# Kernel optimization log

Hardware: AMD Instinct MI355X
Metric: run time of the kernel (lower is better)

## Reference

```python
import jax, jax.numpy as jnp
import numpy as np

B, S = 4096, 4096
NEG_INF = -1e30


def _conv1d_same(x, w, pad):
    # x: [B, S], w: [K] -> cross-correlation with zero padding, like torch F.conv1d
    out = jax.lax.conv_general_dilated(
        x[:, None, :], w[None, None, :], (1,), [(pad, pad)],
        dimension_numbers=("NCH", "OIH", "NCH"))
    return out[:, 0, :]


def setup_inputs() -> dict:
    key = jax.random.key(0)
    kx, kl, k1, k2, k3 = jax.random.split(key, 5)
    x = jax.random.normal(kx, (B, S), dtype=jnp.float32)
    length = jax.random.randint(kl, (B,), 1, S + 1, dtype=jnp.int32)
    w1 = 0.01 * jax.random.normal(k1, (3,), dtype=jnp.float32)
    w2 = 0.01 * jax.random.normal(k2, (5,), dtype=jnp.float32)
    w3 = 0.01 * jax.random.normal(k3, (7,), dtype=jnp.float32)
    return {"x": x, "length": length, "w1": w1, "w2": w2, "w3": w3}


def reference(x, length, w1, w2, w3):
    # mask out padding beyond each sample's length; zeroing x beyond length makes
    # the 'same'-padded conv identical to per-sample conv on the truncated sequence
    pos = jnp.arange(S)
    mask = pos[None, :] < length[:, None]          # [B, S]
    xm = jnp.where(mask, x, 0.0)

    def branch(w, pad):
        logits = _conv1d_same(xm, w, pad)          # [B, S]
        logits = jnp.where(mask, logits, NEG_INF)  # softmax only over valid positions
        qw = jax.nn.softmax(logits, axis=-1)
        return jnp.sum(qw * xm, axis=-1)           # [B]

    s1 = branch(w1, 1)
    s2 = branch(w2, 2)
    s3 = branch(w3, 3)
    fused = (s1 + s2 + s3) / 3.0
    return fused[:, None]                          # [B, 1]
```

## Files before the change

kernel.cpp:

```cpp
#include <hip/hip_runtime.h>

#define SEQ 4096
#define NTHREADS 256

__global__ __launch_bounds__(NTHREADS) void msr_kernel(
    const float* __restrict__ x, const int* __restrict__ length,
    const float* __restrict__ w1, const float* __restrict__ w2,
    const float* __restrict__ w3, float* __restrict__ out)
{
    __shared__ float sm[SEQ + 8];
    __shared__ float red[4][8];

    const int row = blockIdx.x;
    const int tid = threadIdx.x;
    const int L   = length[row];

    const float a0 = w1[0], a1 = w1[1], a2 = w1[2];
    const float b0 = w2[0], b1 = w2[1], b2 = w2[2], b3 = w2[3], b4 = w2[4];
    const float c0 = w3[0], c1 = w3[1], c2 = w3[2], c3 = w3[3],
                c4 = w3[4], c5 = w3[5], c6 = w3[6];

    if (tid < 4) { sm[tid] = 0.0f; sm[4 + SEQ + tid] = 0.0f; }

    const float4* xrow = reinterpret_cast<const float4*>(x + (size_t)row * SEQ);
    for (int q = tid; q < SEQ / 4; q += NTHREADS) {
        const int e = q * 4;
        float4 v;
        if (e + 3 < L) {
            v = xrow[q];
        } else if (e < L) {
            v = xrow[q];
            if (e + 1 >= L) v.y = 0.0f;
            if (e + 2 >= L) v.z = 0.0f;
            v.w = 0.0f;
        } else {
            v = make_float4(0.0f, 0.0f, 0.0f, 0.0f);
        }
        *reinterpret_cast<float4*>(&sm[4 + e]) = v;
    }
    __syncthreads();

    float d1 = 0.f, n1 = 0.f, d2 = 0.f, n2 = 0.f, d3 = 0.f, n3 = 0.f;
    for (int i = tid; i < L; i += NTHREADS) {
        const float* p = &sm[4 + i];
        const float vm3 = p[-3], vm2 = p[-2], vm1 = p[-1], v0 = p[0],
                    vp1 = p[1],  vp2 = p[2],  vp3 = p[3];
        const float l1 = a0*vm1 + a1*v0 + a2*vp1;
        const float l2 = b0*vm2 + b1*vm1 + b2*v0 + b3*vp1 + b4*vp2;
        const float l3 = c0*vm3 + c1*vm2 + c2*vm1 + c3*v0 + c4*vp1 + c5*vp2 + c6*vp3;
        const float e1 = __expf(l1), e2 = __expf(l2), e3 = __expf(l3);
        d1 += e1; n1 = fmaf(e1, v0, n1);
        d2 += e2; n2 = fmaf(e2, v0, n2);
        d3 += e3; n3 = fmaf(e3, v0, n3);
    }

    #pragma unroll
    for (int off = 32; off > 0; off >>= 1) {
        d1 += __shfl_down(d1, off);
        n1 += __shfl_down(n1, off);
        d2 += __shfl_down(d2, off);
        n2 += __shfl_down(n2, off);
        d3 += __shfl_down(d3, off);
        n3 += __shfl_down(n3, off);
    }
    const int wave = tid >> 6;
    const int lane = tid & 63;
    if (lane == 0) {
        red[wave][0] = d1; red[wave][1] = n1; red[wave][2] = d2;
        red[wave][3] = n2; red[wave][4] = d3; red[wave][5] = n3;
    }
    __syncthreads();
    if (tid == 0) {
        float D1 = 0.f, N1 = 0.f, D2 = 0.f, N2 = 0.f, D3 = 0.f, N3 = 0.f;
        #pragma unroll
        for (int w = 0; w < NTHREADS / 64; ++w) {
            D1 += red[w][0]; N1 += red[w][1]; D2 += red[w][2];
            N2 += red[w][3]; D3 += red[w][4]; N3 += red[w][5];
        }
        const float s1 = N1 / D1, s2 = N2 / D2, s3 = N3 / D3;
        out[row] = (s1 + s2 + s3) * (1.0f / 3.0f);
    }
}

extern "C" void kernel_launch(void* const* d_in, const int* in_sizes, int n_in,
                              void* d_out, int out_size, void* d_ws, size_t ws_size,
                              hipStream_t stream) {
    const float* x      = (const float*)d_in[0];
    const int*   length = (const int*)d_in[1];
    const float* w1     = (const float*)d_in[2];
    const float* w2     = (const float*)d_in[3];
    const float* w3     = (const float*)d_in[4];
    float*       out    = (float*)d_out;
    const int    Bn     = in_sizes[1];
    msr_kernel<<<Bn, NTHREADS, 0, stream>>>(x, length, w1, w2, w3, out);
}
```

Measured before the change: 21.96 us.

## Use one wavefront per row with register stencil via lane shuffles

Replaces the 256-thread block that staged the row in LDS with a single 64-lane wave per row that streams 256-element chunks in registers. Conv halos are exchanged with lane shuffles and carried between chunks, and loads are software-pipelined two chunks ahead. Full chunks skip masking, and the shared-memory reduction and barriers go away. In exchange each row is now handled serially by one wave, which lowers per-row parallelism and leans on memory-level parallelism across many small blocks.

New measurement: 21.53 us. 2.0% less time.

```diff
diff --git a/kernel.cpp b/kernel.cpp
--- a/kernel.cpp
+++ b/kernel.cpp
@@ -1,84 +1,107 @@
 #include <hip/hip_runtime.h>
+#include <type_traits>
 
 #define SEQ 4096
-#define NTHREADS 256
+#define CHUNK 256
 
-__global__ __launch_bounds__(NTHREADS) void msr_kernel(
+__global__ __launch_bounds__(64) void msr_kernel(
     const float* __restrict__ x, const int* __restrict__ length,
     const float* __restrict__ w1, const float* __restrict__ w2,
     const float* __restrict__ w3, float* __restrict__ out)
 {
-    __shared__ float sm[SEQ + 8];
-    __shared__ float red[4][8];
+    const int row  = blockIdx.x;
+    const int lane = threadIdx.x & 63;
+    const int L    = length[row];
 
-    const int row = blockIdx.x;
-    const int tid = threadIdx.x;
-    const int L   = length[row];
+    const float a0=w1[0],a1=w1[1],a2=w1[2];
+    const float b0=w2[0],b1=w2[1],b2=w2[2],b3=w2[3],b4=w2[4];
+    const float c0=w3[0],c1=w3[1],c2=w3[2],c3=w3[3],c4=w3[4],c5=w3[5],c6=w3[6];
 
-    const float a0 = w1[0], a1 = w1[1], a2 = w1[2];
-    const float b0 = w2[0], b1 = w2[1], b2 = w2[2], b3 = w2[3], b4 = w2[4];
-    const float c0 = w3[0], c1 = w3[1], c2 = w3[2], c3 = w3[3],
-                c4 = w3[4], c5 = w3[5], c6 = w3[6];
+    const float4* __restrict__ xrow =
+        reinterpret_cast<const float4*>(x + (size_t)row * SEQ);
 
-    if (tid < 4) { sm[tid] = 0.0f; sm[4 + SEQ + tid] = 0.0f; }
+    float d1=0.f,n1=0.f,d2=0.f,n2=0.f,d3=0.f,n3=0.f;
+    float cax=0.f, cay=0.f, caz=0.f;
 
-    const float4* xrow = reinterpret_cast<const float4*>(x + (size_t)row * SEQ);
-    for (int q = tid; q < SEQ / 4; q += NTHREADS) {
-        const int e = q * 4;
-        float4 v;
-        if (e + 3 < L) {
-            v = xrow[q];
-        } else if (e < L) {
-            v = xrow[q];
-            if (e + 1 >= L) v.y = 0.0f;
-            if (e + 2 >= L) v.z = 0.0f;
-            v.w = 0.0f;
-        } else {
-            v = make_float4(0.0f, 0.0f, 0.0f, 0.0f);
+    auto load_chunk = [&](int it) -> float4 {
+        float4 v = make_float4(0.f,0.f,0.f,0.f);
+        const int start = it * CHUNK;
+        if (start < L) {
+            if (start + CHUNK <= L) {
+                v = xrow[(it << 6) + lane];
+            } else {
+                const int e = start + (lane << 2);
+                if (e < L) {
+                    v = xrow[(it << 6) + lane];
+                    if (e + 1 >= L) v.y = 0.f;
+                    if (e + 2 >= L) v.z = 0.f;
+                    if (e + 3 >= L) v.w = 0.f;
+                }
+            }
         }
-        *reinterpret_cast<float4*>(&sm[4 + e]) = v;
+        return v;
+    };
+
+    auto process = [&](const float4 v, const float4 vnext, int ebase, auto MASKED) {
+        constexpr bool M = decltype(MASKED)::value;
+        float Lm3 = __shfl_up(v.y, 1);
+        float Lm2 = __shfl_up(v.z, 1);
+        float Lm1 = __shfl_up(v.w, 1);
+        if (lane == 0) { Lm3 = cax; Lm2 = cay; Lm1 = caz; }
+        float Rp1 = __shfl_down(v.x, 1);
+        float Rp2 = __shfl_down(v.y, 1);
+        float Rp3 = __shfl_down(v.z, 1);
+        const float nb0 = __shfl(vnext.x, 0);
+        const float nb1 = __shfl(vnext.y, 0);
+        const float nb2 = __shfl(vnext.z, 0);
+        if (lane == 63) { Rp1 = nb0; Rp2 = nb1; Rp3 = nb2; }
+
+        const float s[10] = {Lm3, Lm2, Lm1, v.x, v.y, v.z, v.w, Rp1, Rp2, Rp3};
+        #pragma unroll
+        for (int j = 0; j < 4; ++j) {
+            const float xm3=s[j], xm2=s[j+1], xm1=s[j+2], x0=s[j+3],
+                        xp1=s[j+4], xp2=s[j+5], xp3=s[j+6];
+            const float l1 = fmaf(a0,xm1, fmaf(a1,x0, a2*xp1));
+            const float l2 = fmaf(b0,xm2, fmaf(b1,xm1, fmaf(b2,x0,
+                             fmaf(b3,xp1, b4*xp2))));
+            const float l3 = fmaf(c0,xm3, fmaf(c1,xm2, fmaf(c2,xm1, fmaf(c3,x0,
+                             fmaf(c4,xp1, fmaf(c5,xp2, c6*xp3))))));
+            float E1 = __expf(l1), E2 = __expf(l2), E3 = __expf(l3);
+            if (M) {
+                const float msk = (ebase + (lane << 2) + j < L) ? 1.f : 0.f;
+                E1 *= msk; E2 *= msk; E3 *= msk;
+            }
+            d1 += E1; n1 = fmaf(E1, x0, n1);
+            d2 += E2; n2 = fmaf(E2, x0, n2);
+            d3 += E3; n3 = fmaf(E3, x0, n3);
+        }
+        cax = __shfl(v.y, 63);
+        cay = __shfl(v.z, 63);
+        caz = __shfl(v.w, 63);
+    };
+
+    const int  nfull       = L >> 8;
+    const bool has_partial = (L & (CHUNK - 1)) != 0;
+
+    float4 vA = load_chunk(0);
+    float4 vB = load_chunk(1);
+    for (int it = 0; it < nfull; ++it) {
+        float4 vC = load_chunk(it + 2);
+        process(vA, vB, it * CHUNK, std::false_type{});
+        vA = vB; vB = vC;
     }
-    __syncthreads();
-
-    float d1 = 0.f, n1 = 0.f, d2 = 0.f, n2 = 0.f, d3 = 0.f, n3 = 0.f;
-    for (int i = tid; i < L; i += NTHREADS) {
-        const float* p = &sm[4 + i];
-        const float vm3 = p[-3], vm2 = p[-2], vm1 = p[-1], v0 = p[0],
-                    vp1 = p[1],  vp2 = p[2],  vp3 = p[3];
-        const float l1 = a0*vm1 + a1*v0 + a2*vp1;
-        const float l2 = b0*vm2 + b1*vm1 + b2*v0 + b3*vp1 + b4*vp2;
-        const float l3 = c0*vm3 + c1*vm2 + c2*vm1 + c3*v0 + c4*vp1 + c5*vp2 + c6*vp3;
-        const float e1 = __expf(l1), e2 = __expf(l2), e3 = __expf(l3);
-        d1 += e1; n1 = fmaf(e1, v0, n1);
-        d2 += e2; n2 = fmaf(e2, v0, n2);
-        d3 += e3; n3 = fmaf(e3, v0, n3);
+    if (has_partial) {
+        process(vA, vB, nfull * CHUNK, std::true_type{});
     }
 
     #pragma unroll
     for (int off = 32; off > 0; off >>= 1) {
-        d1 += __shfl_down(d1, off);
-        n1 += __shfl_down(n1, off);
-        d2 += __shfl_down(d2, off);
-        n2 += __shfl_down(n2, off);
-        d3 += __shfl_down(d3, off);
-        n3 += __shfl_down(n3, off);
+        d1 += __shfl_xor(d1, off); n1 += __shfl_xor(n1, off);
+        d2 += __shfl_xor(d2, off); n2 += __shfl_xor(n2, off);
+        d3 += __shfl_xor(d3, off); n3 += __shfl_xor(n3, off);
     }
-    const int wave = tid >> 6;
-    const int lane = tid & 63;
     if (lane == 0) {
-        red[wave][0] = d1; red[wave][1] = n1; red[wave][2] = d2;
-        red[wave][3] = n2; red[wave][4] = d3; red[wave][5] = n3;
-    }
-    __syncthreads();
-    if (tid == 0) {
-        float D1 = 0.f, N1 = 0.f, D2 = 0.f, N2 = 0.f, D3 = 0.f, N3 = 0.f;
-        #pragma unroll
-        for (int w = 0; w < NTHREADS / 64; ++w) {
-            D1 += red[w][0]; N1 += red[w][1]; D2 += red[w][2];
-            N2 += red[w][3]; D3 += red[w][4]; N3 += red[w][5];
-        }
-        const float s1 = N1 / D1, s2 = N2 / D2, s3 = N3 / D3;
-        out[row] = (s1 + s2 + s3) * (1.0f / 3.0f);
+        out[row] = (n1/d1 + n2/d2 + n3/d3) * (1.0f/3.0f);
     }
 }
 
@@ -92,5 +115,5 @@
     const float* w3     = (const float*)d_in[4];
     float*       out    = (float*)d_out;
     const int    Bn     = in_sizes[1];
-    msr_kernel<<<Bn, NTHREADS, 0, stream>>>(x, length, w1, w2, w3, out);
+    msr_kernel<<<Bn, 64, 0, stream>>>(x, length, w1, w2, w3, out);
 }
```
